# Kernel optimization log

Measured on AMD Instinct MI355X. Metric: run time of the kernel, lower is better.

Reference implementation:

```python
import jax, jax.numpy as jnp
import numpy as np


def butterfly_mult(twiddle, x):
    # twiddle: (S, M, n//2, 2, 2); x: (B, S, n); increasing_stride=True
    B, S, n = x.shape
    M = twiddle.shape[1]
    out = x
    for idx in range(M):  # loop over log2(n) stages (structural, not data dim)
        stride = 1 << idx
        g = n // (2 * stride)
        t = twiddle[:, idx].reshape(S, g, stride, 2, 2)   # (S, g, r, i, j)
        xr = out.reshape(B, S, g, 2, stride)              # (B, S, g, j, r)
        out = jnp.einsum('sgrij,bsgjr->bsgir', t, xr).reshape(B, S, n)
    return out


def butterfly_layer(x, twiddle, bias, out_size):
    # x: (..., n) with n a power of 2 (pre_process pad is a no-op)
    lead = x.shape[:-1]
    n = x.shape[-1]
    S = twiddle.shape[0]
    xb = x.reshape(-1, n)
    xb = jnp.broadcast_to(xb[:, None, :], (xb.shape[0], S, n))  # expand to nstacks
    out = butterfly_mult(twiddle, xb)
    out = out.reshape(out.shape[0], S * n)[:, :out_size] + bias[:out_size]
    return out.reshape(*lead, out_size)


def setup_inputs() -> dict:
    key = jax.random.key(0)
    ks = jax.random.split(key, 5)
    B, T, D, H = 4, 4096, 1024, 4096
    inv_sqrt2 = 1.0 / np.sqrt(2.0).astype(np.float32)
    x = jax.random.normal(ks[0], (B, T, D), jnp.float32)
    tw1 = jax.random.normal(ks[1], (4, 10, 512, 2, 2), jnp.float32) * inv_sqrt2
    b1 = jax.random.normal(ks[2], (H,), jnp.float32) * 0.02
    tw2 = jax.random.normal(ks[3], (1, 11, 1024, 2, 2), jnp.float32) * inv_sqrt2
    b2 = jax.random.normal(ks[4], (D,), jnp.float32) * 0.02
    return {"x": x, "tw1": tw1, "b1": b1, "tw2": tw2, "b2": b2}


def reference(x, tw1, b1, tw2, b2):
    # GLU: fc1 (butterfly) -> chunk -> x * sigmoid(gates) -> fc2 (butterfly)
    h = butterfly_layer(x, tw1, b1, 4096)      # (B, T, 4096)
    a, gates = jnp.split(h, 2, axis=-1)        # (B, T, 2048) each
    h = a * jax.nn.sigmoid(gates)
    return butterfly_layer(h, tw2, b2, 1024)   # (B, T, 1024)
```

## Files before the change

### kernel.cpp

```cpp
#include <hip/hip_runtime.h>
#include <cstdint>


typedef float          v4f __attribute__((ext_vector_type(4)));
typedef unsigned int   u4i __attribute__((ext_vector_type(4)));
typedef unsigned int   u2i __attribute__((ext_vector_type(2)));
typedef short          bf8 __attribute__((ext_vector_type(8)));

#define MFMA16(A, B, C) __builtin_amdgcn_mfma_f32_16x16x32_bf16(A, B, C, 0, 0, 0)

__device__ __forceinline__ unsigned pk2(float a, float b) {
    unsigned ua = __float_as_uint(a) + 0x8000u;
    unsigned ub = __float_as_uint(b) + 0x8000u;
    return __builtin_amdgcn_perm(ub, ua, 0x07060302u);
}

__device__ __forceinline__ v4f ub4(u2i u) {
    v4f r;
    r.x = __uint_as_float(u.x << 16); r.y = __uint_as_float(u.x & 0xffff0000u);
    r.z = __uint_as_float(u.y << 16); r.w = __uint_as_float(u.y & 0xffff0000u);
    return r;
}

__device__ __forceinline__ float sigmf(float g) {
    return __builtin_amdgcn_rcpf(1.0f + __expf(-g));
}
__device__ __forceinline__ v4f sig4(v4f g) {
    v4f r; r.x = sigmf(g.x); r.y = sigmf(g.y); r.z = sigmf(g.z); r.w = sigmf(g.w);
    return r;
}

__device__ __forceinline__ int ab16(int row, int hw) {
    return (row << 11) + (((hw) << 1) ^ ((row & 7) << 4));
}

struct MP { const float* twf; int np, rbase, rstep, j0; };
__device__ __forceinline__ MP mparams(int mid, const float* tw1, const float* tw2) {
    MP p;
    if (mid < 128)      { p.twf = tw1 + (mid >> 5) * 20480;         p.np = 512;  p.rbase = (mid & 31) * 32; p.rstep = 1;  p.j0 = 0; }
    else if (mid < 256) { p.twf = tw1 + ((mid - 128) >> 5) * 20480; p.np = 512;  p.rbase = mid & 31;        p.rstep = 32; p.j0 = 5; }
    else if (mid < 320) { p.twf = tw2; p.np = 1024; p.rbase = (mid - 256) * 32; p.rstep = 1;  p.j0 = 0; }
    else                { p.twf = tw2; p.np = 1024;
                          p.rbase = (mid & 31) + (((mid - 320) >> 5) << 10);    p.rstep = 32; p.j0 = 5; }
    return p;
}

__global__ void build_mats(const float* __restrict__ tw1,
                           const float* __restrict__ tw2,
                           unsigned short* __restrict__ wsm)
{
    __shared__ v4f   tlds[160];
    __shared__ float slds[64];
    const int t = threadIdx.x;
    const int midb = blockIdx.x * 2;

    #pragma unroll
    for (int qq = 0; qq < 3; ++qq) {
        const int q = t + qq * 64;
        if (q < 160) {
            const int ml = (q >= 80) ? 1 : 0, rem = q - ml * 80;
            const int jj = rem >> 4, pr = rem & 15;
            const MP p = mparams(midb + ml, tw1, tw2);
            const int j  = p.j0 + jj;
            const int r0 = ((pr >> jj) << (jj + 1)) | (pr & ((1 << jj) - 1));
            const int pp = p.rbase + r0 * p.rstep;
            const int tidx = ((pp >> (j + 1)) << j) | (pp & ((1 << j) - 1));
            tlds[q] = *(const v4f*)(p.twf + (size_t)(j * p.np + tidx) * 4);
        }
    }
    {
        const int ml = t >> 5, r = t & 31, mid = midb + ml;
        if (mid >= 320) {
            const int l2s = mid & 31, sb = (mid - 320) >> 5;
            slds[t] = tw2[(size_t)(10 * 1024 + l2s + 32 * r) * 4 + sb];
        }
    }
    __syncthreads();

    const int ml = t >> 5, c = t & 31, mid = midb + ml;
    float v[32];
    #pragma unroll
    for (int r = 0; r < 32; ++r) v[r] = (r == c) ? 1.0f : 0.0f;

    #pragma unroll
    for (int jj = 0; jj < 5; ++jj) {
        #pragma unroll
        for (int pr = 0; pr < 16; ++pr) {
            const int r0 = ((pr >> jj) << (jj + 1)) | (pr & ((1 << jj) - 1));
            const int r1 = r0 | (1 << jj);
            const v4f T  = tlds[ml * 80 + jj * 16 + pr];
            const float a = v[r0], b = v[r1];
            v[r0] = T.x * a + T.y * b;
            v[r1] = T.z * a + T.w * b;
        }
    }
    if (mid >= 320) {
        #pragma unroll
        for (int r = 0; r < 32; ++r) v[r] *= slds[ml * 32 + r];
    }
    #pragma unroll
    for (int r = 0; r < 32; ++r) {
        const int mt   = r >> 4;
        const int lane = (r & 15) + ((c >> 3) << 4);
        wsm[((size_t)(mid * 2 + mt) * 64 + lane) * 8 + (c & 7)] =
            (unsigned short)((__float_as_uint(v[r]) + 0x8000u) >> 16);
    }
}

__global__ __launch_bounds__(512, 4) void glu_bfly(
    const float* __restrict__ x, const float* __restrict__ b1,
    const float* __restrict__ b2, const bf8* __restrict__ mats,
    float* __restrict__ out)
{
    extern __shared__ char lds[];
    char*           actA  = lds;
    char*           actB  = lds + 32768;
    unsigned short* b1t16 = (unsigned short*)(lds + 65536);

    const int t = threadIdx.x, w = t >> 6, l = t & 63, lr = l & 15, lk = l >> 4;
    const int row0 = blockIdx.x * 16;
    const v4f vz = {0.f, 0.f, 0.f, 0.f};

    {
        const v4f* bp = (const v4f*)(b1 + t * 8);
        const v4f a = bp[0], b = bp[1];
        const float vals[8] = {a.x, a.y, a.z, a.w, b.x, b.y, b.z, b.w};
        #pragma unroll
        for (int k = 0; k < 8; ++k) {
            const int gid = t * 8 + k, s = gid >> 10, r = gid & 1023;
            b1t16[(s << 10) + ((r & 31) << 5) + (r >> 5)] =
                (unsigned short)((__float_as_uint(vals[k]) + 0x8000u) >> 16);
        }
    }

    bf8 xf[4];
    #pragma unroll
    for (int gi = 0; gi < 4; ++gi) {
        const float* xp = x + (size_t)(row0 + lr) * 1024 + (w * 4 + gi) * 32 + lk * 8;
        const v4f a = *(const v4f*)xp, b = *(const v4f*)(xp + 4);
        u4i uu; uu.x = pk2(a.x, a.y); uu.y = pk2(a.z, a.w);
        uu.z = pk2(b.x, b.y); uu.w = pk2(b.z, b.w);
        xf[gi] = __builtin_bit_cast(bf8, uu);
    }

    unsigned z0p[4][2][2];
    v4f fin[4][2];

    #pragma unroll
    for (int h = 0; h < 2; ++h) {
        const int sa = h, sg = h + 2;

        #pragma unroll
        for (int pass = 0; pass < 2; ++pass) {
            const int s = pass ? sg : sa;
            char* dst = pass ? actB : actA;
            v4f acc[2][4];
            __builtin_amdgcn_s_setprio(1);
            #pragma unroll
            for (int mt = 0; mt < 2; ++mt)
            #pragma unroll
            for (int gi = 0; gi < 4; ++gi) {
                const bf8 am = mats[((s * 32 + w * 4 + gi) * 2 + mt) * 64 + l];
                acc[mt][gi] = MFMA16(am, xf[gi], vz);
            }
            __builtin_amdgcn_s_setprio(0);
            #pragma unroll
            for (int mt = 0; mt < 2; ++mt)
            #pragma unroll
            for (int rg = 0; rg < 4; ++rg) {
                const int m = mt * 16 + lk * 4 + rg;
                u2i pv;
                pv.x = pk2(acc[mt][0][rg], acc[mt][1][rg]);
                pv.y = pk2(acc[mt][2][rg], acc[mt][3][rg]);
                *(u2i*)(dst + ab16(lr, 32 * m + 4 * w)) = pv;
            }
            __syncthreads();
        }

        {
            v4f uacc[4][2];
            #pragma unroll
            for (int li = 0; li < 4; ++li) {
                const int lg = w * 4 + li;
                const bf8 fa = *(const bf8*)(actA + ab16(lr, 32 * lg + 8 * lk));
                const bf8 fg = *(const bf8*)(actB + ab16(lr, 32 * lg + 8 * lk));
                const int mida = 128 + sa * 32 + lg, midg = 128 + sg * 32 + lg;
                const bf8 aa0 = mats[(mida * 2 + 0) * 64 + l];
                const bf8 aa1 = mats[(mida * 2 + 1) * 64 + l];
                const bf8 ag0 = mats[(midg * 2 + 0) * 64 + l];
                const bf8 ag1 = mats[(midg * 2 + 1) * 64 + l];
                __builtin_amdgcn_s_setprio(1);
                const v4f ha0 = MFMA16(aa0, fa, vz), ha1 = MFMA16(aa1, fa, vz);
                const v4f hg0 = MFMA16(ag0, fg, vz), hg1 = MFMA16(ag1, fg, vz);
                __builtin_amdgcn_s_setprio(0);
                const int bia = ((sa * 32 + lg) << 5) + lk * 4;
                const int big = ((sg * 32 + lg) << 5) + lk * 4;
                const v4f ba0 = ub4(*(const u2i*)&b1t16[bia]);
                const v4f ba1 = ub4(*(const u2i*)&b1t16[bia + 16]);
                const v4f bg0 = ub4(*(const u2i*)&b1t16[big]);
                const v4f bg1 = ub4(*(const u2i*)&b1t16[big + 16]);
                uacc[li][0] = (ha0 + ba0) * sig4(hg0 + bg0);
                uacc[li][1] = (ha1 + ba1) * sig4(hg1 + bg1);
            }
            __syncthreads();
            #pragma unroll
            for (int mt = 0; mt < 2; ++mt)
            #pragma unroll
            for (int rg = 0; rg < 4; ++rg) {
                const int m = mt * 16 + lk * 4 + rg;
                u2i pv;
                pv.x = pk2(uacc[0][mt][rg], uacc[1][mt][rg]);
                pv.y = pk2(uacc[2][mt][rg], uacc[3][mt][rg]);
                *(u2i*)(actA + ab16(lr, 32 * m + 4 * w)) = pv;
            }
            __syncthreads();
        }

        {
            v4f acc[2][4];
            #pragma unroll
            for (int gi = 0; gi < 4; ++gi) {
                const int g = w * 4 + gi, mid = 256 + 32 * h + g;
                const bf8 f  = *(const bf8*)(actA + ab16(lr, 32 * g + 8 * lk));
                const bf8 a0 = mats[(mid * 2 + 0) * 64 + l];
                const bf8 a1 = mats[(mid * 2 + 1) * 64 + l];
                __builtin_amdgcn_s_setprio(1);
                acc[0][gi] = MFMA16(a0, f, vz);
                acc[1][gi] = MFMA16(a1, f, vz);
                __builtin_amdgcn_s_setprio(0);
            }
            #pragma unroll
            for (int mt = 0; mt < 2; ++mt)
            #pragma unroll
            for (int rg = 0; rg < 4; ++rg) {
                const int m = mt * 16 + lk * 4 + rg;
                u2i pv;
                pv.x = pk2(acc[mt][0][rg], acc[mt][1][rg]);
                pv.y = pk2(acc[mt][2][rg], acc[mt][3][rg]);
                *(u2i*)(actB + ab16(lr, 32 * m + 4 * w)) = pv;
            }
            __syncthreads();
        }

        #pragma unroll
        for (int li = 0; li < 4; ++li) {
            const int lg = w * 4 + li, mid = 320 + 32 * h + lg;
            const bf8 f  = *(const bf8*)(actB + ab16(lr, 32 * lg + 8 * lk));
            const bf8 a0 = mats[(mid * 2 + 0) * 64 + l];
            const bf8 a1 = mats[(mid * 2 + 1) * 64 + l];
            __builtin_amdgcn_s_setprio(1);
            const v4f z0 = MFMA16(a0, f, vz);
            const v4f z1 = MFMA16(a1, f, vz);
            __builtin_amdgcn_s_setprio(0);
            if (h == 0) {
                z0p[li][0][0] = pk2(z0.x, z0.y); z0p[li][0][1] = pk2(z0.z, z0.w);
                z0p[li][1][0] = pk2(z1.x, z1.y); z0p[li][1][1] = pk2(z1.z, z1.w);
            } else {
                u2i u0; u0.x = z0p[li][0][0]; u0.y = z0p[li][0][1];
                u2i u1; u1.x = z0p[li][1][0]; u1.y = z0p[li][1][1];
                fin[li][0] = z0 + ub4(u0);
                fin[li][1] = z1 + ub4(u1);
            }
        }
    }

    __syncthreads();
    #pragma unroll
    for (int mt = 0; mt < 2; ++mt)
    #pragma unroll
    for (int rg = 0; rg < 4; ++rg) {
        const int p0 = 4 * w + 32 * (mt * 16 + lk * 4 + rg);
        v4f vv;
        vv.x = fin[0][mt][rg]; vv.y = fin[1][mt][rg];
        vv.z = fin[2][mt][rg]; vv.w = fin[3][mt][rg];
        *(v4f*)(lds + (lr << 12) + ((p0 << 2) ^ ((lr & 7) << 4))) = vv;
    }
    __syncthreads();
    {
        const int row = t >> 5, c0 = (t & 31) * 4;
        #pragma unroll
        for (int i = 0; i < 8; ++i) {
            const int col = c0 + 128 * i;
            v4f ov = *(const v4f*)(lds + (row << 12) + ((col << 2) ^ ((row & 7) << 4)));
            ov += *(const v4f*)(b2 + col);
            *(v4f*)(out + (size_t)(row0 + row) * 1024 + col) = ov;
        }
    }
}

extern "C" void kernel_launch(void* const* d_in, const int* in_sizes, int n_in,
                              void* d_out, int out_size, void* d_ws, size_t ws_size,
                              hipStream_t stream) {
    const float* x   = (const float*)d_in[0];
    const float* tw1 = (const float*)d_in[1];
    const float* b1  = (const float*)d_in[2];
    const float* tw2 = (const float*)d_in[3];
    const float* b2  = (const float*)d_in[4];

    build_mats<<<192, 64, 0, stream>>>(tw1, tw2, (unsigned short*)d_ws);

    (void)hipFuncSetAttribute((const void*)glu_bfly,
                              hipFuncAttributeMaxDynamicSharedMemorySize, 73728);
    glu_bfly<<<1024, 512, 73728, stream>>>(x, b1, b2, (const bf8*)d_ws,
                                           (float*)d_out);
}
```

Before: 158.6 us.

## Process 32 rows per block to reuse butterfly matrices and prefetch weights

New measurement: 154.5 us. 2.6% less time.

```diff
diff --git a/kernel.cpp b/kernel.cpp
--- a/kernel.cpp
+++ b/kernel.cpp
@@ -8,6 +8,12 @@
 typedef short          bf8 __attribute__((ext_vector_type(8)));
 
 #define MFMA16(A, B, C) __builtin_amdgcn_mfma_f32_16x16x32_bf16(A, B, C, 0, 0, 0)
+
+#define BAR() do {                                          \
+    asm volatile("s_waitcnt lgkmcnt(0)" ::: "memory");      \
+    __builtin_amdgcn_s_barrier();                           \
+    asm volatile("" ::: "memory");                          \
+} while (0)
 
 __device__ __forceinline__ unsigned pk2(float a, float b) {
     unsigned ua = __float_as_uint(a) + 0x8000u;
@@ -30,7 +36,7 @@
     return r;
 }
 
-__device__ __forceinline__ int ab16(int row, int hw) {
+__device__ __forceinline__ int ab(int row, int hw) {
     return (row << 11) + (((hw) << 1) ^ ((row & 7) << 4));
 }
 
@@ -49,8 +55,9 @@
                            const float* __restrict__ tw2,
                            unsigned short* __restrict__ wsm)
 {
-    __shared__ v4f   tlds[160];
-    __shared__ float slds[64];
+    __shared__ v4f            tlds[160];
+    __shared__ float          slds[64];
+    __shared__ unsigned short obuf[2048];
     const int t = threadIdx.x;
     const int midb = blockIdx.x * 2;
 
@@ -69,7 +76,7 @@
         }
     }
     {
-        const int ml = t >> 5, r = t & 31, mid = midb + ml;
+        const int ml2 = t >> 5, r = t & 31, mid = midb + ml2;
         if (mid >= 320) {
             const int l2s = mid & 31, sb = (mid - 320) >> 5;
             slds[t] = tw2[(size_t)(10 * 1024 + l2s + 32 * r) * 4 + sb];
@@ -102,23 +109,30 @@
     for (int r = 0; r < 32; ++r) {
         const int mt   = r >> 4;
         const int lane = (r & 15) + ((c >> 3) << 4);
-        wsm[((size_t)(mid * 2 + mt) * 64 + lane) * 8 + (c & 7)] =
+        obuf[((ml * 2 + mt) * 64 + lane) * 8 + (c & 7)] =
             (unsigned short)((__float_as_uint(v[r]) + 0x8000u) >> 16);
     }
-}
-
-__global__ __launch_bounds__(512, 4) void glu_bfly(
+    __syncthreads();
+    {
+        const u4i* ob = (const u4i*)obuf;
+        u4i* gb = (u4i*)(wsm + (size_t)midb * 1024);
+        #pragma unroll
+        for (int k = 0; k < 4; ++k) gb[t * 4 + k] = ob[t * 4 + k];
+    }
+}
+
+__global__ __launch_bounds__(512, 2) void glu_bfly(
     const float* __restrict__ x, const float* __restrict__ b1,
     const float* __restrict__ b2, const bf8* __restrict__ mats,
     float* __restrict__ out)
 {
     extern __shared__ char lds[];
     char*           actA  = lds;
-    char*           actB  = lds + 32768;
-    unsigned short* b1t16 = (unsigned short*)(lds + 65536);
+    char*           actB  = lds + 65536;
+    unsigned short* b1t16 = (unsigned short*)(lds + 131072);
 
     const int t = threadIdx.x, w = t >> 6, l = t & 63, lr = l & 15, lk = l >> 4;
-    const int row0 = blockIdx.x * 16;
+    const int row0 = blockIdx.x * 32;
     const v4f vz = {0.f, 0.f, 0.f, 0.f};
 
     {
@@ -133,158 +147,247 @@
         }
     }
 
-    bf8 xf[4];
-    #pragma unroll
-    for (int gi = 0; gi < 4; ++gi) {
-        const float* xp = x + (size_t)(row0 + lr) * 1024 + (w * 4 + gi) * 32 + lk * 8;
+    bf8 xf[4][2];
+    #pragma unroll
+    for (int gi = 0; gi < 4; ++gi)
+    #pragma unroll
+    for (int nh = 0; nh < 2; ++nh) {
+        const float* xp = x + (size_t)(row0 + nh * 16 + lr) * 1024 + (w * 4 + gi) * 32 + lk * 8;
         const v4f a = *(const v4f*)xp, b = *(const v4f*)(xp + 4);
         u4i uu; uu.x = pk2(a.x, a.y); uu.y = pk2(a.z, a.w);
         uu.z = pk2(b.x, b.y); uu.w = pk2(b.z, b.w);
-        xf[gi] = __builtin_bit_cast(bf8, uu);
-    }
-
-    unsigned z0p[4][2][2];
-    v4f fin[4][2];
+        xf[gi][nh] = __builtin_bit_cast(bf8, uu);
+    }
+
+    unsigned z0p[4][2][2][2];
+    v4f fin[4][2][2];
+
+    bf8 m1a[8];
+    #pragma unroll
+    for (int q = 0; q < 8; ++q)
+        m1a[q] = mats[((0 * 32 + w * 4 + (q >> 1)) * 2 + (q & 1)) * 64 + l];
 
     #pragma unroll
     for (int h = 0; h < 2; ++h) {
         const int sa = h, sg = h + 2;
 
-        #pragma unroll
-        for (int pass = 0; pass < 2; ++pass) {
-            const int s = pass ? sg : sa;
-            char* dst = pass ? actB : actA;
-            v4f acc[2][4];
+        bf8 m1b[8];
+        #pragma unroll
+        for (int q = 0; q < 8; ++q)
+            m1b[q] = mats[((sg * 32 + w * 4 + (q >> 1)) * 2 + (q & 1)) * 64 + l];
+        {
+            v4f acc[4][2][2];
             __builtin_amdgcn_s_setprio(1);
             #pragma unroll
-            for (int mt = 0; mt < 2; ++mt)
-            #pragma unroll
-            for (int gi = 0; gi < 4; ++gi) {
-                const bf8 am = mats[((s * 32 + w * 4 + gi) * 2 + mt) * 64 + l];
-                acc[mt][gi] = MFMA16(am, xf[gi], vz);
+            for (int gi = 0; gi < 4; ++gi)
+            #pragma unroll
+            for (int nh = 0; nh < 2; ++nh) {
+                acc[gi][nh][0] = MFMA16(m1a[gi * 2 + 0], xf[gi][nh], vz);
+                acc[gi][nh][1] = MFMA16(m1a[gi * 2 + 1], xf[gi][nh], vz);
             }
             __builtin_amdgcn_s_setprio(0);
+            #pragma unroll
+            for (int nh = 0; nh < 2; ++nh)
             #pragma unroll
             for (int mt = 0; mt < 2; ++mt)
             #pragma unroll
             for (int rg = 0; rg < 4; ++rg) {
                 const int m = mt * 16 + lk * 4 + rg;
                 u2i pv;
-                pv.x = pk2(acc[mt][0][rg], acc[mt][1][rg]);
-                pv.y = pk2(acc[mt][2][rg], acc[mt][3][rg]);
-                *(u2i*)(dst + ab16(lr, 32 * m + 4 * w)) = pv;
-            }
-            __syncthreads();
-        }
-
+                pv.x = pk2(acc[0][nh][mt][rg], acc[1][nh][mt][rg]);
+                pv.y = pk2(acc[2][nh][mt][rg], acc[3][nh][mt][rg]);
+                *(u2i*)(actA + ab(nh * 16 + lr, 32 * m + 4 * w)) = pv;
+            }
+        }
         {
-            v4f uacc[4][2];
-            #pragma unroll
-            for (int li = 0; li < 4; ++li) {
-                const int lg = w * 4 + li;
-                const bf8 fa = *(const bf8*)(actA + ab16(lr, 32 * lg + 8 * lk));
-                const bf8 fg = *(const bf8*)(actB + ab16(lr, 32 * lg + 8 * lk));
-                const int mida = 128 + sa * 32 + lg, midg = 128 + sg * 32 + lg;
-                const bf8 aa0 = mats[(mida * 2 + 0) * 64 + l];
-                const bf8 aa1 = mats[(mida * 2 + 1) * 64 + l];
-                const bf8 ag0 = mats[(midg * 2 + 0) * 64 + l];
-                const bf8 ag1 = mats[(midg * 2 + 1) * 64 + l];
-                __builtin_amdgcn_s_setprio(1);
-                const v4f ha0 = MFMA16(aa0, fa, vz), ha1 = MFMA16(aa1, fa, vz);
-                const v4f hg0 = MFMA16(ag0, fg, vz), hg1 = MFMA16(ag1, fg, vz);
-                __builtin_amdgcn_s_setprio(0);
-                const int bia = ((sa * 32 + lg) << 5) + lk * 4;
-                const int big = ((sg * 32 + lg) << 5) + lk * 4;
-                const v4f ba0 = ub4(*(const u2i*)&b1t16[bia]);
-                const v4f ba1 = ub4(*(const u2i*)&b1t16[bia + 16]);
-                const v4f bg0 = ub4(*(const u2i*)&b1t16[big]);
-                const v4f bg1 = ub4(*(const u2i*)&b1t16[big + 16]);
-                uacc[li][0] = (ha0 + ba0) * sig4(hg0 + bg0);
-                uacc[li][1] = (ha1 + ba1) * sig4(hg1 + bg1);
-            }
-            __syncthreads();
+            v4f acc[4][2][2];
+            __builtin_amdgcn_s_setprio(1);
+            #pragma unroll
+            for (int gi = 0; gi < 4; ++gi)
+            #pragma unroll
+            for (int nh = 0; nh < 2; ++nh) {
+                acc[gi][nh][0] = MFMA16(m1b[gi * 2 + 0], xf[gi][nh], vz);
+                acc[gi][nh][1] = MFMA16(m1b[gi * 2 + 1], xf[gi][nh], vz);
+            }
+            __builtin_amdgcn_s_setprio(0);
+            #pragma unroll
+            for (int nh = 0; nh < 2; ++nh)
             #pragma unroll
             for (int mt = 0; mt < 2; ++mt)
             #pragma unroll
             for (int rg = 0; rg < 4; ++rg) {
                 const int m = mt * 16 + lk * 4 + rg;
                 u2i pv;
-                pv.x = pk2(uacc[0][mt][rg], uacc[1][mt][rg]);
-                pv.y = pk2(uacc[2][mt][rg], uacc[3][mt][rg]);
-                *(u2i*)(actA + ab16(lr, 32 * m + 4 * w)) = pv;
-            }
-            __syncthreads();
-        }
+                pv.x = pk2(acc[0][nh][mt][rg], acc[1][nh][mt][rg]);
+                pv.y = pk2(acc[2][nh][mt][rg], acc[3][nh][mt][rg]);
+                *(u2i*)(actB + ab(nh * 16 + lr, 32 * m + 4 * w)) = pv;
+            }
+        }
+        bf8 cm[4];
+        cm[0] = mats[((128 + sa * 32 + w * 4 + 0) * 2 + 0) * 64 + l];
+        cm[1] = mats[((128 + sa * 32 + w * 4 + 0) * 2 + 1) * 64 + l];
+        cm[2] = mats[((128 + sg * 32 + w * 4 + 0) * 2 + 0) * 64 + l];
+        cm[3] = mats[((128 + sg * 32 + w * 4 + 0) * 2 + 1) * 64 + l];
+        BAR();
+
+        v4f uacc[4][2][2];
+        #pragma unroll
+        for (int li = 0; li < 4; ++li) {
+            bf8 nm[4];
+            if (li < 3) {
+                nm[0] = mats[((128 + sa * 32 + w * 4 + li + 1) * 2 + 0) * 64 + l];
+                nm[1] = mats[((128 + sa * 32 + w * 4 + li + 1) * 2 + 1) * 64 + l];
+                nm[2] = mats[((128 + sg * 32 + w * 4 + li + 1) * 2 + 0) * 64 + l];
+                nm[3] = mats[((128 + sg * 32 + w * 4 + li + 1) * 2 + 1) * 64 + l];
+            }
+            const int lg = w * 4 + li;
+            const bf8 fa0 = *(const bf8*)(actA + ab(lr,      32 * lg + 8 * lk));
+            const bf8 fa1 = *(const bf8*)(actA + ab(16 + lr, 32 * lg + 8 * lk));
+            const bf8 fg0 = *(const bf8*)(actB + ab(lr,      32 * lg + 8 * lk));
+            const bf8 fg1 = *(const bf8*)(actB + ab(16 + lr, 32 * lg + 8 * lk));
+            v4f ha[2][2], hg[2][2];
+            __builtin_amdgcn_s_setprio(1);
+            ha[0][0] = MFMA16(cm[0], fa0, vz); ha[0][1] = MFMA16(cm[1], fa0, vz);
+            ha[1][0] = MFMA16(cm[0], fa1, vz); ha[1][1] = MFMA16(cm[1], fa1, vz);
+            hg[0][0] = MFMA16(cm[2], fg0, vz); hg[0][1] = MFMA16(cm[3], fg0, vz);
+            hg[1][0] = MFMA16(cm[2], fg1, vz); hg[1][1] = MFMA16(cm[3], fg1, vz);
+            __builtin_amdgcn_s_setprio(0);
+            const int bia = ((sa * 32 + lg) << 5) + lk * 4;
+            const int big = ((sg * 32 + lg) << 5) + lk * 4;
+            const v4f ba0 = ub4(*(const u2i*)&b1t16[bia]);
+            const v4f ba1 = ub4(*(const u2i*)&b1t16[bia + 16]);
+            const v4f bg0 = ub4(*(const u2i*)&b1t16[big]);
+            const v4f bg1 = ub4(*(const u2i*)&b1t16[big + 16]);
+            #pragma unroll
+            for (int nh = 0; nh < 2; ++nh) {
+                uacc[li][nh][0] = (ha[nh][0] + ba0) * sig4(hg[nh][0] + bg0);
+                uacc[li][nh][1] = (ha[nh][1] + ba1) * sig4(hg[nh][1] + bg1);
+            }
+            if (li < 3) { cm[0] = nm[0]; cm[1] = nm[1]; cm[2] = nm[2]; cm[3] = nm[3]; }
+        }
+        bf8 m3[8];
+        #pragma unroll
+        for (int q = 0; q < 8; ++q)
+            m3[q] = mats[((256 + 32 * h + w * 4 + (q >> 1)) * 2 + (q & 1)) * 64 + l];
+        BAR();
+        #pragma unroll
+        for (int nh = 0; nh < 2; ++nh)
+        #pragma unroll
+        for (int mt = 0; mt < 2; ++mt)
+        #pragma unroll
+        for (int rg = 0; rg < 4; ++rg) {
+            const int m = mt * 16 + lk * 4 + rg;
+            u2i pv;
+            pv.x = pk2(uacc[0][nh][mt][rg], uacc[1][nh][mt][rg]);
+            pv.y = pk2(uacc[2][nh][mt][rg], uacc[3][nh][mt][rg]);
+            *(u2i*)(actA + ab(nh * 16 + lr, 32 * m + 4 * w)) = pv;
+        }
+        BAR();
 
         {
-            v4f acc[2][4];
+            v4f acc[4][2][2];
             #pragma unroll
             for (int gi = 0; gi < 4; ++gi) {
-                const int g = w * 4 + gi, mid = 256 + 32 * h + g;
-                const bf8 f  = *(const bf8*)(actA + ab16(lr, 32 * g + 8 * lk));
-                const bf8 a0 = mats[(mid * 2 + 0) * 64 + l];
-                const bf8 a1 = mats[(mid * 2 + 1) * 64 + l];
-                __builtin_amdgcn_s_setprio(1);
-                acc[0][gi] = MFMA16(a0, f, vz);
-                acc[1][gi] = MFMA16(a1, f, vz);
-                __builtin_amdgcn_s_setprio(0);
-            }
+                const int g = w * 4 + gi;
+                #pragma unroll
+                for (int nh = 0; nh < 2; ++nh) {
+                    const bf8 f = *(const bf8*)(actA + ab(nh * 16 + lr, 32 * g + 8 * lk));
+                    __builtin_amdgcn_s_setprio(1);
+                    acc[gi][nh][0] = MFMA16(m3[gi * 2 + 0], f, vz);
+                    acc[gi][nh][1] = MFMA16(m3[gi * 2 + 1], f, vz);
+                    __builtin_amdgcn_s_setprio(0);
+                }
+            }
+            bf8 m4p[4];
+            m4p[0] = mats[((320 + 32 * h + w * 4 + 0) * 2 + 0) * 64 + l];
+            m4p[1] = mats[((320 + 32 * h + w * 4 + 0) * 2 + 1) * 64 + l];
+            m4p[2] = mats[((320 + 32 * h + w * 4 + 1) * 2 + 0) * 64 + l];
+            m4p[3] = mats[((320 + 32 * h + w * 4 + 1) * 2 + 1) * 64 + l];
+            #pragma unroll
+            for (int nh = 0; nh < 2; ++nh)
             #pragma unroll
             for (int mt = 0; mt < 2; ++mt)
             #pragma unroll
             for (int rg = 0; rg < 4; ++rg) {
                 const int m = mt * 16 + lk * 4 + rg;
                 u2i pv;
-                pv.x = pk2(acc[mt][0][rg], acc[mt][1][rg]);
-                pv.y = pk2(acc[mt][2][rg], acc[mt][3][rg]);
-                *(u2i*)(actB + ab16(lr, 32 * m + 4 * w)) = pv;
-            }
-            __syncthreads();
-        }
-
-        #pragma unroll
-        for (int li = 0; li < 4; ++li) {
-            const int lg = w * 4 + li, mid = 320 + 32 * h + lg;
-            const bf8 f  = *(const bf8*)(actB + ab16(lr, 32 * lg + 8 * lk));
-            const bf8 a0 = mats[(mid * 2 + 0) * 64 + l];
-            const bf8 a1 = mats[(mid * 2 + 1) * 64 + l];
-            __builtin_amdgcn_s_setprio(1);
-            const v4f z0 = MFMA16(a0, f, vz);
-            const v4f z1 = MFMA16(a1, f, vz);
-            __builtin_amdgcn_s_setprio(0);
-            if (h == 0) {
-                z0p[li][0][0] = pk2(z0.x, z0.y); z0p[li][0][1] = pk2(z0.z, z0.w);
-                z0p[li][1][0] = pk2(z1.x, z1.y); z0p[li][1][1] = pk2(z1.z, z1.w);
-            } else {
-                u2i u0; u0.x = z0p[li][0][0]; u0.y = z0p[li][0][1];
-                u2i u1; u1.x = z0p[li][1][0]; u1.y = z0p[li][1][1];
-                fin[li][0] = z0 + ub4(u0);
-                fin[li][1] = z1 + ub4(u1);
-            }
-        }
-    }
-
-    __syncthreads();
-    #pragma unroll
-    for (int mt = 0; mt < 2; ++mt)
-    #pragma unroll
-    for (int rg = 0; rg < 4; ++rg) {
-        const int p0 = 4 * w + 32 * (mt * 16 + lk * 4 + rg);
-        v4f vv;
-        vv.x = fin[0][mt][rg]; vv.y = fin[1][mt][rg];
-        vv.z = fin[2][mt][rg]; vv.w = fin[3][mt][rg];
-        *(v4f*)(lds + (lr << 12) + ((p0 << 2) ^ ((lr & 7) << 4))) = vv;
-    }
-    __syncthreads();
-    {
-        const int row = t >> 5, c0 = (t & 31) * 4;
-        #pragma unroll
-        for (int i = 0; i < 8; ++i) {
-            const int col = c0 + 128 * i;
-            v4f ov = *(const v4f*)(lds + (row << 12) + ((col << 2) ^ ((row & 7) << 4)));
-            ov += *(const v4f*)(b2 + col);
-            *(v4f*)(out + (size_t)(row0 + row) * 1024 + col) = ov;
-        }
+                pv.x = pk2(acc[0][nh][mt][rg], acc[1][nh][mt][rg]);
+                pv.y = pk2(acc[2][nh][mt][rg], acc[3][nh][mt][rg]);
+                *(u2i*)(actB + ab(nh * 16 + lr, 32 * m + 4 * w)) = pv;
+            }
+            BAR();
+
+            bf8 m4[4];
+            m4[0] = m4p[0]; m4[1] = m4p[1]; m4[2] = m4p[2]; m4[3] = m4p[3];
+            #pragma unroll
+            for (int li = 0; li < 4; ++li) {
+                bf8 n4[2];
+                if (li < 2) {
+                    n4[0] = mats[((320 + 32 * h + w * 4 + li + 2) * 2 + 0) * 64 + l];
+                    n4[1] = mats[((320 + 32 * h + w * 4 + li + 2) * 2 + 1) * 64 + l];
+                }
+                const int lg = w * 4 + li;
+                const bf8 f0 = *(const bf8*)(actB + ab(lr,      32 * lg + 8 * lk));
+                const bf8 f1 = *(const bf8*)(actB + ab(16 + lr, 32 * lg + 8 * lk));
+                v4f zz[2][2];
+                __builtin_amdgcn_s_setprio(1);
+                zz[0][0] = MFMA16(m4[(li & 1) * 2 + 0], f0, vz);
+                zz[0][1] = MFMA16(m4[(li & 1) * 2 + 1], f0, vz);
+                zz[1][0] = MFMA16(m4[(li & 1) * 2 + 0], f1, vz);
+                zz[1][1] = MFMA16(m4[(li & 1) * 2 + 1], f1, vz);
+                __builtin_amdgcn_s_setprio(0);
+                if (h == 0) {
+                    #pragma unroll
+                    for (int nh = 0; nh < 2; ++nh)
+                    #pragma unroll
+                    for (int mt = 0; mt < 2; ++mt) {
+                        z0p[li][nh][mt][0] = pk2(zz[nh][mt].x, zz[nh][mt].y);
+                        z0p[li][nh][mt][1] = pk2(zz[nh][mt].z, zz[nh][mt].w);
+                    }
+                } else {
+                    #pragma unroll
+                    for (int nh = 0; nh < 2; ++nh)
+                    #pragma unroll
+                    for (int mt = 0; mt < 2; ++mt) {
+                        u2i uu; uu.x = z0p[li][nh][mt][0]; uu.y = z0p[li][nh][mt][1];
+                        fin[li][nh][mt] = zz[nh][mt] + ub4(uu);
+                    }
+                }
+                if (li < 2) { m4[(li & 1) * 2 + 0] = n4[0]; m4[(li & 1) * 2 + 1] = n4[1]; }
+            }
+        }
+        if (h == 0) {
+            #pragma unroll
+            for (int q = 0; q < 8; ++q)
+                m1a[q] = mats[((1 * 32 + w * 4 + (q >> 1)) * 2 + (q & 1)) * 64 + l];
+        }
+        BAR();
+    }
+
+    #pragma unroll
+    for (int nh = 0; nh < 2; ++nh) {
+        #pragma unroll
+        for (int mt = 0; mt < 2; ++mt)
+        #pragma unroll
+        for (int rg = 0; rg < 4; ++rg) {
+            const int p0 = 4 * w + 32 * (mt * 16 + lk * 4 + rg);
+            v4f vv;
+            vv.x = fin[0][nh][mt][rg]; vv.y = fin[1][nh][mt][rg];
+            vv.z = fin[2][nh][mt][rg]; vv.w = fin[3][nh][mt][rg];
+            *(v4f*)(lds + (lr << 12) + ((p0 << 2) ^ ((lr & 7) << 4))) = vv;
+        }
+        BAR();
+        {
+            const int row = t >> 5, c0 = (t & 31) * 4;
+            #pragma unroll
+            for (int i = 0; i < 8; ++i) {
+                const int col = c0 + 128 * i;
+                v4f ov = *(const v4f*)(lds + (row << 12) + ((col << 2) ^ ((row & 7) << 4)));
+                ov += *(const v4f*)(b2 + col);
+                *(v4f*)(out + (size_t)(row0 + nh * 16 + row) * 1024 + col) = ov;
+            }
+        }
+        BAR();
     }
 }
 
@@ -300,7 +403,7 @@
     build_mats<<<192, 64, 0, stream>>>(tw1, tw2, (unsigned short*)d_ws);
 
     (void)hipFuncSetAttribute((const void*)glu_bfly,
-                              hipFuncAttributeMaxDynamicSharedMemorySize, 73728);
-    glu_bfly<<<1024, 512, 73728, stream>>>(x, b1, b2, (const bf8*)d_ws,
+                              hipFuncAttributeMaxDynamicSharedMemorySize, 139264);
+    glu_bfly<<<512, 512, 139264, stream>>>(x, b1, b2, (const bf8*)d_ws,
                                            (float*)d_out);
 }
```

## Double-buffer LDS to interleave both GLU halves and cut barriers

Applied to the files above, without the earlier changes.

After: 166.5 us. 1.05x slower.

```diff
diff --git a/kernel.cpp b/kernel.cpp
--- a/kernel.cpp
+++ b/kernel.cpp
@@ -8,6 +8,12 @@
 typedef short          bf8 __attribute__((ext_vector_type(8)));
 
 #define MFMA16(A, B, C) __builtin_amdgcn_mfma_f32_16x16x32_bf16(A, B, C, 0, 0, 0)
+
+#define BAR() do {                                          \
+    asm volatile("s_waitcnt lgkmcnt(0)" ::: "memory");      \
+    __builtin_amdgcn_s_barrier();                           \
+    asm volatile("" ::: "memory");                          \
+} while (0)
 
 __device__ __forceinline__ unsigned pk2(float a, float b) {
     unsigned ua = __float_as_uint(a) + 0x8000u;
@@ -49,8 +55,9 @@
                            const float* __restrict__ tw2,
                            unsigned short* __restrict__ wsm)
 {
-    __shared__ v4f   tlds[160];
-    __shared__ float slds[64];
+    __shared__ v4f            tlds[160];
+    __shared__ float          slds[64];
+    __shared__ unsigned short obuf[2048];
     const int t = threadIdx.x;
     const int midb = blockIdx.x * 2;
 
@@ -69,7 +76,7 @@
         }
     }
     {
-        const int ml = t >> 5, r = t & 31, mid = midb + ml;
+        const int ml2 = t >> 5, r = t & 31, mid = midb + ml2;
         if (mid >= 320) {
             const int l2s = mid & 31, sb = (mid - 320) >> 5;
             slds[t] = tw2[(size_t)(10 * 1024 + l2s + 32 * r) * 4 + sb];
@@ -102,24 +109,34 @@
     for (int r = 0; r < 32; ++r) {
         const int mt   = r >> 4;
         const int lane = (r & 15) + ((c >> 3) << 4);
-        wsm[((size_t)(mid * 2 + mt) * 64 + lane) * 8 + (c & 7)] =
+        obuf[((ml * 2 + mt) * 64 + lane) * 8 + (c & 7)] =
             (unsigned short)((__float_as_uint(v[r]) + 0x8000u) >> 16);
     }
-}
-
-__global__ __launch_bounds__(512, 4) void glu_bfly(
+    __syncthreads();
+    {
+        const u4i* ob = (const u4i*)obuf;
+        u4i* gb = (u4i*)(wsm + (size_t)midb * 1024);
+        #pragma unroll
+        for (int k = 0; k < 4; ++k) gb[t * 4 + k] = ob[t * 4 + k];
+    }
+}
+
+__global__ __launch_bounds__(512, 2) void glu_bfly(
     const float* __restrict__ x, const float* __restrict__ b1,
     const float* __restrict__ b2, const bf8* __restrict__ mats,
     float* __restrict__ out)
 {
     extern __shared__ char lds[];
-    char*           actA  = lds;
-    char*           actB  = lds + 32768;
-    unsigned short* b1t16 = (unsigned short*)(lds + 65536);
+    char* A0 = lds;
+    char* B0 = lds + 32768;
+    char* A1 = lds + 65536;
+    char* B1 = lds + 98304;
+    unsigned short* b1t16 = (unsigned short*)(lds + 131072);
 
     const int t = threadIdx.x, w = t >> 6, l = t & 63, lr = l & 15, lk = l >> 4;
     const int row0 = blockIdx.x * 16;
     const v4f vz = {0.f, 0.f, 0.f, 0.f};
+    const bf8* mp = mats + l;
 
     {
         const v4f* bp = (const v4f*)(b1 + t * 8);
@@ -143,128 +160,128 @@
         xf[gi] = __builtin_bit_cast(bf8, uu);
     }
 
+    v4f uacc0[4][2], uacc1[4][2];
     unsigned z0p[4][2][2];
     v4f fin[4][2];
 
-    #pragma unroll
-    for (int h = 0; h < 2; ++h) {
-        const int sa = h, sg = h + 2;
-
-        #pragma unroll
-        for (int pass = 0; pass < 2; ++pass) {
-            const int s = pass ? sg : sa;
-            char* dst = pass ? actB : actA;
-            v4f acc[2][4];
-            __builtin_amdgcn_s_setprio(1);
-            #pragma unroll
-            for (int mt = 0; mt < 2; ++mt)
-            #pragma unroll
-            for (int gi = 0; gi < 4; ++gi) {
-                const bf8 am = mats[((s * 32 + w * 4 + gi) * 2 + mt) * 64 + l];
-                acc[mt][gi] = MFMA16(am, xf[gi], vz);
-            }
-            __builtin_amdgcn_s_setprio(0);
-            #pragma unroll
-            for (int mt = 0; mt < 2; ++mt)
-            #pragma unroll
-            for (int rg = 0; rg < 4; ++rg) {
-                const int m = mt * 16 + lk * 4 + rg;
-                u2i pv;
-                pv.x = pk2(acc[mt][0][rg], acc[mt][1][rg]);
-                pv.y = pk2(acc[mt][2][rg], acc[mt][3][rg]);
-                *(u2i*)(dst + ab16(lr, 32 * m + 4 * w)) = pv;
-            }
-            __syncthreads();
-        }
-
-        {
-            v4f uacc[4][2];
-            #pragma unroll
-            for (int li = 0; li < 4; ++li) {
-                const int lg = w * 4 + li;
-                const bf8 fa = *(const bf8*)(actA + ab16(lr, 32 * lg + 8 * lk));
-                const bf8 fg = *(const bf8*)(actB + ab16(lr, 32 * lg + 8 * lk));
-                const int mida = 128 + sa * 32 + lg, midg = 128 + sg * 32 + lg;
-                const bf8 aa0 = mats[(mida * 2 + 0) * 64 + l];
-                const bf8 aa1 = mats[(mida * 2 + 1) * 64 + l];
-                const bf8 ag0 = mats[(midg * 2 + 0) * 64 + l];
-                const bf8 ag1 = mats[(midg * 2 + 1) * 64 + l];
-                __builtin_amdgcn_s_setprio(1);
-                const v4f ha0 = MFMA16(aa0, fa, vz), ha1 = MFMA16(aa1, fa, vz);
-                const v4f hg0 = MFMA16(ag0, fg, vz), hg1 = MFMA16(ag1, fg, vz);
-                __builtin_amdgcn_s_setprio(0);
-                const int bia = ((sa * 32 + lg) << 5) + lk * 4;
-                const int big = ((sg * 32 + lg) << 5) + lk * 4;
-                const v4f ba0 = ub4(*(const u2i*)&b1t16[bia]);
-                const v4f ba1 = ub4(*(const u2i*)&b1t16[bia + 16]);
-                const v4f bg0 = ub4(*(const u2i*)&b1t16[big]);
-                const v4f bg1 = ub4(*(const u2i*)&b1t16[big + 16]);
-                uacc[li][0] = (ha0 + ba0) * sig4(hg0 + bg0);
-                uacc[li][1] = (ha1 + ba1) * sig4(hg1 + bg1);
-            }
-            __syncthreads();
-            #pragma unroll
-            for (int mt = 0; mt < 2; ++mt)
-            #pragma unroll
-            for (int rg = 0; rg < 4; ++rg) {
-                const int m = mt * 16 + lk * 4 + rg;
-                u2i pv;
-                pv.x = pk2(uacc[0][mt][rg], uacc[1][mt][rg]);
-                pv.y = pk2(uacc[2][mt][rg], uacc[3][mt][rg]);
-                *(u2i*)(actA + ab16(lr, 32 * m + 4 * w)) = pv;
-            }
-            __syncthreads();
-        }
-
-        {
-            v4f acc[2][4];
-            #pragma unroll
-            for (int gi = 0; gi < 4; ++gi) {
-                const int g = w * 4 + gi, mid = 256 + 32 * h + g;
-                const bf8 f  = *(const bf8*)(actA + ab16(lr, 32 * g + 8 * lk));
-                const bf8 a0 = mats[(mid * 2 + 0) * 64 + l];
-                const bf8 a1 = mats[(mid * 2 + 1) * 64 + l];
-                __builtin_amdgcn_s_setprio(1);
-                acc[0][gi] = MFMA16(a0, f, vz);
-                acc[1][gi] = MFMA16(a1, f, vz);
-                __builtin_amdgcn_s_setprio(0);
-            }
-            #pragma unroll
-            for (int mt = 0; mt < 2; ++mt)
-            #pragma unroll
-            for (int rg = 0; rg < 4; ++rg) {
-                const int m = mt * 16 + lk * 4 + rg;
-                u2i pv;
-                pv.x = pk2(acc[mt][0][rg], acc[mt][1][rg]);
-                pv.y = pk2(acc[mt][2][rg], acc[mt][3][rg]);
-                *(u2i*)(actB + ab16(lr, 32 * m + 4 * w)) = pv;
-            }
-            __syncthreads();
-        }
-
+    auto S1 = [&](int s, char* dst) {
+        v4f acc[2][4];
+        #pragma unroll
+        for (int mt = 0; mt < 2; ++mt)
+        #pragma unroll
+        for (int gi = 0; gi < 4; ++gi) {
+            const bf8 am = mp[((s * 32 + w * 4 + gi) * 2 + mt) * 64];
+            acc[mt][gi] = MFMA16(am, xf[gi], vz);
+        }
+        #pragma unroll
+        for (int mt = 0; mt < 2; ++mt)
+        #pragma unroll
+        for (int rg = 0; rg < 4; ++rg) {
+            const int m = mt * 16 + lk * 4 + rg;
+            u2i pv;
+            pv.x = pk2(acc[mt][0][rg], acc[mt][1][rg]);
+            pv.y = pk2(acc[mt][2][rg], acc[mt][3][rg]);
+            *(u2i*)(dst + ab16(lr, 32 * m + 4 * w)) = pv;
+        }
+    };
+
+    auto S2 = [&](int h, char* A, char* B, v4f (&uacc)[4][2]) {
         #pragma unroll
         for (int li = 0; li < 4; ++li) {
-            const int lg = w * 4 + li, mid = 320 + 32 * h + lg;
-            const bf8 f  = *(const bf8*)(actB + ab16(lr, 32 * lg + 8 * lk));
-            const bf8 a0 = mats[(mid * 2 + 0) * 64 + l];
-            const bf8 a1 = mats[(mid * 2 + 1) * 64 + l];
-            __builtin_amdgcn_s_setprio(1);
-            const v4f z0 = MFMA16(a0, f, vz);
-            const v4f z1 = MFMA16(a1, f, vz);
-            __builtin_amdgcn_s_setprio(0);
-            if (h == 0) {
-                z0p[li][0][0] = pk2(z0.x, z0.y); z0p[li][0][1] = pk2(z0.z, z0.w);
-                z0p[li][1][0] = pk2(z1.x, z1.y); z0p[li][1][1] = pk2(z1.z, z1.w);
-            } else {
-                u2i u0; u0.x = z0p[li][0][0]; u0.y = z0p[li][0][1];
-                u2i u1; u1.x = z0p[li][1][0]; u1.y = z0p[li][1][1];
-                fin[li][0] = z0 + ub4(u0);
-                fin[li][1] = z1 + ub4(u1);
-            }
-        }
-    }
-
-    __syncthreads();
+            const int lg = w * 4 + li;
+            const bf8 fa = *(const bf8*)(A + ab16(lr, 32 * lg + 8 * lk));
+            const bf8 fg = *(const bf8*)(B + ab16(lr, 32 * lg + 8 * lk));
+            const int mida = 128 + h * 32 + lg, midg = 128 + (h + 2) * 32 + lg;
+            const bf8 aa0 = mp[(mida * 2 + 0) * 64];
+            const bf8 aa1 = mp[(mida * 2 + 1) * 64];
+            const bf8 ag0 = mp[(midg * 2 + 0) * 64];
+            const bf8 ag1 = mp[(midg * 2 + 1) * 64];
+            const v4f ha0 = MFMA16(aa0, fa, vz), ha1 = MFMA16(aa1, fa, vz);
+            const v4f hg0 = MFMA16(ag0, fg, vz), hg1 = MFMA16(ag1, fg, vz);
+            const int bia = ((h * 32 + lg) << 5) + lk * 4;
+            const int big = (((h + 2) * 32 + lg) << 5) + lk * 4;
+            const v4f ba0 = ub4(*(const u2i*)&b1t16[bia]);
+            const v4f ba1 = ub4(*(const u2i*)&b1t16[bia + 16]);
+            const v4f bg0 = ub4(*(const u2i*)&b1t16[big]);
+            const v4f bg1 = ub4(*(const u2i*)&b1t16[big + 16]);
+            uacc[li][0] = (ha0 + ba0) * sig4(hg0 + bg0);
+            uacc[li][1] = (ha1 + ba1) * sig4(hg1 + bg1);
+        }
+    };
+
+    auto S3 = [&](char* A, const v4f (&uacc)[4][2]) {
+        #pragma unroll
+        for (int mt = 0; mt < 2; ++mt)
+        #pragma unroll
+        for (int rg = 0; rg < 4; ++rg) {
+            const int m = mt * 16 + lk * 4 + rg;
+            u2i pv;
+            pv.x = pk2(uacc[0][mt][rg], uacc[1][mt][rg]);
+            pv.y = pk2(uacc[2][mt][rg], uacc[3][mt][rg]);
+            *(u2i*)(A + ab16(lr, 32 * m + 4 * w)) = pv;
+        }
+    };
+
+    auto S4 = [&](int h, char* A, char* B) {
+        v4f acc[2][4];
+        #pragma unroll
+        for (int gi = 0; gi < 4; ++gi) {
+            const int g = w * 4 + gi, mid = 256 + 32 * h + g;
+            const bf8 f  = *(const bf8*)(A + ab16(lr, 32 * g + 8 * lk));
+            const bf8 a0 = mp[(mid * 2 + 0) * 64];
+            const bf8 a1 = mp[(mid * 2 + 1) * 64];
+            acc[0][gi] = MFMA16(a0, f, vz);
+            acc[1][gi] = MFMA16(a1, f, vz);
+        }
+        #pragma unroll
+        for (int mt = 0; mt < 2; ++mt)
+        #pragma unroll
+        for (int rg = 0; rg < 4; ++rg) {
+            const int m = mt * 16 + lk * 4 + rg;
+            u2i pv;
+            pv.x = pk2(acc[mt][0][rg], acc[mt][1][rg]);
+            pv.y = pk2(acc[mt][2][rg], acc[mt][3][rg]);
+            *(u2i*)(B + ab16(lr, 32 * m + 4 * w)) = pv;
+        }
+    };
+
+    S1(0, A0); S1(2, B0);
+    BAR();
+    S2(0, A0, B0, uacc0);
+    S1(1, A1); S1(3, B1);
+    BAR();
+    S3(A0, uacc0);
+    S2(1, A1, B1, uacc1);
+    BAR();
+    S4(0, A0, B0);
+    S3(A1, uacc1);
+    BAR();
+    #pragma unroll
+    for (int li = 0; li < 4; ++li) {
+        const int lg = w * 4 + li, mid = 320 + 0 + lg;
+        const bf8 f  = *(const bf8*)(B0 + ab16(lr, 32 * lg + 8 * lk));
+        const bf8 a0 = mp[(mid * 2 + 0) * 64];
+        const bf8 a1 = mp[(mid * 2 + 1) * 64];
+        const v4f z0 = MFMA16(a0, f, vz);
+        const v4f z1 = MFMA16(a1, f, vz);
+        z0p[li][0][0] = pk2(z0.x, z0.y); z0p[li][0][1] = pk2(z0.z, z0.w);
+        z0p[li][1][0] = pk2(z1.x, z1.y); z0p[li][1][1] = pk2(z1.z, z1.w);
+    }
+    S4(1, A1, B1);
+    BAR();
+    #pragma unroll
+    for (int li = 0; li < 4; ++li) {
+        const int lg = w * 4 + li, mid = 320 + 32 + lg;
+        const bf8 f  = *(const bf8*)(B1 + ab16(lr, 32 * lg + 8 * lk));
+        const bf8 a0 = mp[(mid * 2 + 0) * 64];
+        const bf8 a1 = mp[(mid * 2 + 1) * 64];
+        const v4f z0 = MFMA16(a0, f, vz);
+        const v4f z1 = MFMA16(a1, f, vz);
+        u2i u0; u0.x = z0p[li][0][0]; u0.y = z0p[li][0][1];
+        u2i u1; u1.x = z0p[li][1][0]; u1.y = z0p[li][1][1];
+        fin[li][0] = z0 + ub4(u0);
+        fin[li][1] = z1 + ub4(u1);
+    }
     #pragma unroll
     for (int mt = 0; mt < 2; ++mt)
     #pragma unroll
@@ -275,7 +292,7 @@
         vv.z = fin[2][mt][rg]; vv.w = fin[3][mt][rg];
         *(v4f*)(lds + (lr << 12) + ((p0 << 2) ^ ((lr & 7) << 4))) = vv;
     }
-    __syncthreads();
+    BAR();
     {
         const int row = t >> 5, c0 = (t & 31) * 4;
         #pragma unroll
@@ -300,7 +317,7 @@
     build_mats<<<192, 64, 0, stream>>>(tw1, tw2, (unsigned short*)d_ws);
 
     (void)hipFuncSetAttribute((const void*)glu_bfly,
-                              hipFuncAttributeMaxDynamicSharedMemorySize, 73728);
-    glu_bfly<<<1024, 512, 73728, stream>>>(x, b1, b2, (const bf8*)d_ws,
-                                           (float*)d_out);
-}
+                              hipFuncAttributeMaxDynamicSharedMemorySize, 139264);
+    glu_bfly<<<1024, 512, 139264, stream>>>(x, b1, b2, (const bf8*)d_ws,
+                                            (float*)d_out);
+}
```
